# Kernel optimization log

Hardware: AMD Instinct MI355X
Metric: run time of the kernel (lower is better)

## Reference

```python
import jax, jax.numpy as jnp
import numpy as np

B, C, H, W = 2, 192, 48, 512
EMB, HEADS, DOUT, MAXM, THR, EPS = 64, 2, 192, 64, 0.01, 1e-5
DV = DOUT // HEADS  # per-head value dim (96)


def setup_inputs() -> dict:
    key = jax.random.key(0)
    ks = jax.random.split(key, 16)
    s = 0.02
    inp = {
        "l": jax.random.normal(ks[0], (B, C, H, W), jnp.float32),
        "r": jax.random.normal(ks[1], (B, C, H, W), jnp.float32),
        "ln_l_g": jnp.ones((C,), jnp.float32),
        "ln_l_b": jnp.zeros((C,), jnp.float32),
        "ln_r_g": jnp.ones((C,), jnp.float32),
        "ln_r_b": jnp.zeros((C,), jnp.float32),
    }
    ki = 2
    for p in ("rtl", "ltr"):
        inp[p + "_wq"] = jax.random.normal(ks[ki], (HEADS * EMB, C, 3), jnp.float32) * s; ki += 1
        inp[p + "_bq"] = jnp.zeros((HEADS * EMB,), jnp.float32)
        inp[p + "_wk"] = jax.random.normal(ks[ki], (HEADS * EMB, C, 3), jnp.float32) * s; ki += 1
        inp[p + "_bk"] = jnp.zeros((HEADS * EMB,), jnp.float32)
        inp[p + "_wv"] = jax.random.normal(ks[ki], (DOUT, C, 3), jnp.float32) * s; ki += 1
        inp[p + "_bv"] = jnp.zeros((DOUT,), jnp.float32)
        inp[p + "_wo"] = jax.random.normal(ks[ki], (DOUT, DOUT), jnp.float32) * s; ki += 1
        inp[p + "_bo"] = jnp.zeros((DOUT,), jnp.float32)
    inp["ffl_w"] = jax.random.normal(ks[ki], (DOUT, DOUT), jnp.float32) * s; ki += 1
    inp["ffl_b"] = jnp.zeros((DOUT,), jnp.float32)
    inp["ffr_w"] = jax.random.normal(ks[ki], (DOUT, DOUT), jnp.float32) * s; ki += 1
    inp["ffr_b"] = jnp.zeros((DOUT,), jnp.float32)
    return inp


def _layernorm(x, g, b):
    m = x.mean(-1, keepdims=True)
    v = x.var(-1, keepdims=True)
    return (x - m) / jnp.sqrt(v + EPS) * g + b


def _conv1d(x, w, b):
    # x: [N, Cin, L], w: [Cout, Cin, 3], same padding
    y = jax.lax.conv_general_dilated(x, w, (1,), [(1, 1)], dimension_numbers=("NCH", "OIH", "NCH"))
    return y + b[None, :, None]


def _conv_attn(q_seq, k_seq, v_seq, wq, bq, wk, bk, wv, bv, wo, bo, mask):
    # q_seq/k_seq/v_seq: [N, L, C]; mask: [L, L] bool (True = masked)
    N, L, _ = q_seq.shape
    Q = _conv1d(q_seq.transpose(0, 2, 1), wq, bq).reshape(N, HEADS, EMB, L).transpose(0, 1, 3, 2)  # b h l d
    K = _conv1d(k_seq.transpose(0, 2, 1), wk, bk).reshape(N, HEADS, EMB, L).transpose(0, 1, 3, 2)
    V = _conv1d(v_seq.transpose(0, 2, 1), wv, bv).reshape(N, HEADS, DV, L).transpose(0, 1, 3, 2)
    A = jnp.einsum("bhqd,bhkd->bhqk", Q, K) / np.sqrt(EMB).astype(np.float32)
    A = jnp.where(mask, -jnp.inf, A)
    A = jax.nn.softmax(A, axis=-1)
    A = A * (A > THR)  # valid_mask thresholding after softmax
    O = jnp.einsum("bhqk,bhkd->bhqd", A, V)
    O = O.transpose(0, 2, 1, 3).reshape(N, L, DOUT)
    return jnp.einsum("nld,od->nlo", O, wo) + bo, A


def reference(l, r, ln_l_g, ln_l_b, ln_r_g, ln_r_b,
              rtl_wq, rtl_bq, rtl_wk, rtl_bk, rtl_wv, rtl_bv, rtl_wo, rtl_bo,
              ltr_wq, ltr_bq, ltr_wk, ltr_bk, ltr_wv, ltr_bv, ltr_wo, ltr_bo,
              ffl_w, ffl_b, ffr_w, ffr_b):
    ls = l.transpose(0, 2, 3, 1).reshape(B * H, W, C)  # (b h) w c
    rs = r.transpose(0, 2, 3, 1).reshape(B * H, W, C)
    ln_ = _layernorm(ls, ln_l_g, ln_l_b)
    rn_ = _layernorm(rs, ln_r_g, ln_r_b)
    i = jnp.arange(W)[:, None]
    j = jnp.arange(W)[None, :]
    mask_left = (j < i) | (j - i > MAXM)   # left query i attends keys j in [i, i+MAXM]
    mask_right = (j > i) | (i - j > MAXM)  # right query i attends keys j in [i-MAXM, i]
    l_mha, A_rtl = _conv_attn(ln_, rn_, rs, rtl_wq, rtl_bq, rtl_wk, rtl_bk, rtl_wv, rtl_bv, rtl_wo, rtl_bo, mask_left)
    r_mha, A_ltr = _conv_attn(rn_, ln_, ls, ltr_wq, ltr_bq, ltr_wk, ltr_bk, ltr_wv, ltr_bv, ltr_wo, ltr_bo, mask_right)
    lo = ls + l_mha
    ro = rs + r_mha
    lo = lo + (jnp.einsum("nwc,oc->nwo", lo, ffl_w) + ffl_b)
    ro = ro + (jnp.einsum("nwc,oc->nwo", ro, ffr_w) + ffr_b)
    l_out = lo.reshape(B, H, W, C).transpose(0, 3, 1, 2)
    r_out = ro.reshape(B, H, W, C).transpose(0, 3, 1, 2)
    return (l_out, r_out, A_rtl, A_ltr)
```

## Files before the change

kernel.cpp:

```cpp
#include <hip/hip_runtime.h>
#include <cstddef>
#include <cstdint>

constexpr int kC = 192;
constexpr int kW = 512;
constexpr int kHH = 48;

typedef unsigned short u16;
typedef __attribute__((ext_vector_type(8))) short bf16x8;
typedef __attribute__((ext_vector_type(4))) float f32x4;
typedef __attribute__((ext_vector_type(4))) unsigned short us4;

__device__ inline u16 f2bf(float f) {
  union { float f; uint32_t u; } v; v.f = f;
  uint32_t r = v.u + 0x7FFF + ((v.u >> 16) & 1);
  return (u16)(r >> 16);
}
__device__ inline float bf2f(u16 u) {
  return __uint_as_float(((uint32_t)u) << 16);
}

__global__ void __launch_bounds__(256) prep_kernel(
    const float* __restrict__ xl, const float* __restrict__ xr,
    const float* __restrict__ gl, const float* __restrict__ bl,
    const float* __restrict__ gr, const float* __restrict__ br,
    u16* __restrict__ lnl, u16* __restrict__ lraw,
    u16* __restrict__ lnr, u16* __restrict__ rraw,
    const float* wq0, const float* wk0, const float* wv0,
    const float* wq1, const float* wk1, const float* wv1,
    const float* bq0, const float* bk0, const float* bv0,
    const float* bq1, const float* bk1, const float* bv1,
    const float* wo0, const float* wo1, const float* fw0, const float* fw1,
    u16* __restrict__ wall, u16* __restrict__ pfw, float* __restrict__ ball) {
  int bid = blockIdx.x;
  int tid = threadIdx.x;
  if (bid >= 1536) {
    int idx = (bid - 1536) * 256 + tid;
    if (idx < 516096) {
      int dir = idx / 258048, off = idx % 258048;
      const float* src; int soff;
      if (off < 73728) { src = dir ? wq1 : wq0; soff = off; }
      else if (off < 147456) { src = dir ? wk1 : wk0; soff = off - 73728; }
      else { src = dir ? wv1 : wv0; soff = off - 147456; }
      int o = soff / 576, k = soff % 576, t = k / 192, c = k % 192;
      wall[idx] = f2bf(src[((size_t)o * kC + c) * 3 + t]);
    } else if (idx < 516096 + 147456) {
      int i2 = idx - 516096;
      int mat = i2 / 36864, off = i2 % 36864;
      const float* src = mat == 0 ? wo0 : mat == 1 ? wo1 : mat == 2 ? fw0 : fw1;
      pfw[i2] = f2bf(src[off]);
    } else if (idx < 516096 + 147456 + 896) {
      int bi = idx - 516096 - 147456;
      int dir = bi / 448, boff = bi % 448;
      const float* s; int so;
      if (boff < 128) { s = dir ? bq1 : bq0; so = boff; }
      else if (boff < 256) { s = dir ? bk1 : bk0; so = boff - 128; }
      else { s = dir ? bv1 : bv0; so = boff - 256; }
      ball[bi] = s[so];
    }
    return;
  }
  int w0 = (bid & 7) * 64;
  int n = (bid >> 3) % 96;
  int side = bid / 768;
  const float* x = side ? xr : xl;
  const float* g = side ? gr : gl;
  const float* b = side ? br : bl;
  u16* lnout = side ? lnr : lnl;
  u16* rawout = side ? rraw : lraw;
  int bb = n / kHH, h = n % kHH;
  __shared__ float tile[64][193];
  __shared__ float red[8][64];
  __shared__ float mean_s[64], rstd_s[64];
  int lane = tid & 63, wv = tid >> 6;
  for (int c = wv; c < kC; c += 4)
    tile[lane][c] = x[(((size_t)bb * kC + c) * kHH + h) * kW + w0 + lane];
  __syncthreads();
  {
    int w = tid & 63, part = tid >> 6;
    float s = 0.f, s2 = 0.f;
    const float* row = &tile[w][0];
    for (int c = part * 48; c < part * 48 + 48; ++c) {
      float v = row[c];
      s += v; s2 += v * v;
    }
    red[part][w] = s;
    red[part + 4][w] = s2;
  }
  __syncthreads();
  if (tid < 64) {
    float s = red[0][tid] + red[1][tid] + red[2][tid] + red[3][tid];
    float s2 = red[4][tid] + red[5][tid] + red[6][tid] + red[7][tid];
    float m = s * (1.f / 192.f);
    float var = s2 * (1.f / 192.f) - m * m;
    mean_s[tid] = m;
    rstd_s[tid] = rsqrtf(var + 1e-5f);
  }
  __syncthreads();
  for (int u = tid; u < 64 * 48; u += 256) {
    int w = u / 48, c4 = (u % 48) * 4;
    float mm = mean_s[w], rs = rstd_s[w];
    us4 lp, rp;
#pragma unroll
    for (int j = 0; j < 4; ++j) {
      float raw = tile[w][c4 + j];
      rp[j] = f2bf(raw);
      lp[j] = f2bf((raw - mm) * rs * g[c4 + j] + b[c4 + j]);
    }
    size_t idx = ((size_t)n * kW + w0 + w) * kC + c4;
    *reinterpret_cast<us4*>(&lnout[idx]) = lp;
    *reinterpret_cast<us4*>(&rawout[idx]) = rp;
  }
}

template <int NF>
__device__ __forceinline__ void conv_core(
    const u16* __restrict__ in, const u16* __restrict__ w2,
    int n, int l0, u16* As, f32x4 (&acc)[4][NF]) {
  int tid = threadIdx.x;
  int wid = tid >> 6, lane = tid & 63;
  int wm = wid >> 1, wn = wid & 1;
  int lr = lane & 15, g = lane >> 4;
  for (int u = tid; u < 130 * 48; u += 256) {
    int row = u / 48, q = u % 48;
    int l = l0 - 1 + row;
    us4 v = {0, 0, 0, 0};
    if (l >= 0 && l < kW)
      v = *reinterpret_cast<const us4*>(in + ((size_t)n * kW + l) * kC + q * 4);
    *reinterpret_cast<us4*>(&As[row * 200 + q * 4]) = v;
  }
  __syncthreads();
  const u16* wbase = w2 + (size_t)(wn * NF * 16 + lr) * 576 + g * 8;
#pragma unroll
  for (int t = 0; t < 3; ++t) {
#pragma unroll
    for (int c0 = 0; c0 < 192; c0 += 64) {
#pragma unroll
      for (int ks = 0; ks < 2; ++ks) {
        bf16x8 a[4], b[NF];
#pragma unroll
        for (int mf = 0; mf < 4; ++mf)
          a[mf] = *reinterpret_cast<const bf16x8*>(
              &As[(wm * 64 + mf * 16 + lr + t) * 200 + c0 + ks * 32 + g * 8]);
#pragma unroll
        for (int nf = 0; nf < NF; ++nf)
          b[nf] = *reinterpret_cast<const bf16x8*>(
              wbase + (size_t)nf * 16 * 576 + t * 192 + c0 + ks * 32);
#pragma unroll
        for (int mf = 0; mf < 4; ++mf)
#pragma unroll
          for (int nf = 0; nf < NF; ++nf)
            acc[mf][nf] = __builtin_amdgcn_mfma_f32_16x16x32_bf16(a[mf], b[nf], acc[mf][nf], 0, 0, 0);
      }
    }
  }
}

__global__ void __launch_bounds__(256) conv_qk(
    const u16* __restrict__ lnl, const u16* __restrict__ lnr,
    const u16* __restrict__ wall, const float* __restrict__ ball,
    u16* __restrict__ Qbf, u16* __restrict__ Kbf, float* __restrict__ A0) {
  if (blockIdx.y == 4) {
    int fid = blockIdx.z * 4 + blockIdx.x;
    int base_row = fid * 256;
    f32x4 z4 = {0.f, 0.f, 0.f, 0.f};
    for (int u = threadIdx.x; u < 256 * 128; u += 256) {
      int lrow = u >> 7, c4 = u & 127;
      int rg = base_row + lrow;
      int nh = rg >> 9, i = rg & 511;
      int q0 = i & ~63;
      int w1 = q0 + 128 > 512 ? 512 : q0 + 128;
      int col = c4 * 4;
      if (col < q0 || col >= w1)
        __builtin_nontemporal_store(z4, reinterpret_cast<f32x4*>(
            A0 + (size_t)nh * 262144 + (size_t)i * 512 + col));
    }
    return;
  }
  int l0 = blockIdx.x * 128;
  int jid = blockIdx.y;
  int n = blockIdx.z;
  int dir = jid >> 1, which = jid & 1;
  const u16* in = which == 0 ? (dir ? lnr : lnl) : (dir ? lnl : lnr);
  const u16* w2 = wall + (size_t)dir * 258048 + which * 73728;
  const float* bias = ball + dir * 448 + which * 128;

  __shared__ __attribute__((aligned(16))) u16 As[130 * 200];
  f32x4 acc[4][4] = {};
  conv_core<4>(in, w2, n, l0, As, acc);

  int tid = threadIdx.x;
  int wid = tid >> 6, lane = tid & 63;
  int wm = wid >> 1, wn = wid & 1;
  int lr = lane & 15, g = lane >> 4;
  __syncthreads();
  u16* Ts = As;
#pragma unroll
  for (int nf = 0; nf < 4; ++nf) {
    int o = wn * 64 + nf * 16 + lr;
    float bsv = bias[o];
#pragma unroll
    for (int mf = 0; mf < 4; ++mf) {
      int lbase = wm * 64 + mf * 16 + g * 4;
#pragma unroll
      for (int rg = 0; rg < 4; ++rg)
        Ts[(lbase + rg) * 132 + o] = f2bf(acc[mf][nf][rg] + bsv);
    }
  }
  __syncthreads();
  u16* outp = (which == 0 ? Qbf : Kbf) + (size_t)dir * 6291456;
  for (int u = tid; u < 4096; u += 256) {
    int hh = u >> 11;
    int rem = u & 2047;
    int l = rem >> 4, q4 = (rem & 15) * 4;
    us4 v = *reinterpret_cast<const us4*>(&Ts[l * 132 + hh * 64 + q4]);
    *reinterpret_cast<us4*>(
        &outp[((size_t)(n * 2 + hh) * kW + l0 + l) * 64 + q4]) = v;
  }
}

__global__ void __launch_bounds__(256) conv_v(
    const u16* __restrict__ lraw, const u16* __restrict__ rraw,
    const u16* __restrict__ wall, const float* __restrict__ ball,
    u16* __restrict__ Vbf, float* __restrict__ A1) {
  if (blockIdx.y == 2) {
    int fid = blockIdx.z * 4 + blockIdx.x;
    int base_row = fid * 256;
    f32x4 z4 = {0.f, 0.f, 0.f, 0.f};
    for (int u = threadIdx.x; u < 256 * 128; u += 256) {
      int lrow = u >> 7, c4 = u & 127;
      int rg = base_row + lrow;
      int nh = rg >> 9, i = rg & 511;
      int q0 = i & ~63;
      int w0 = q0 >= 64 ? q0 - 64 : 0;
      int col = c4 * 4;
      if (col < w0 || col >= q0 + 64)
        __builtin_nontemporal_store(z4, reinterpret_cast<f32x4*>(
            A1 + (size_t)nh * 262144 + (size_t)i * 512 + col));
    }
    return;
  }
  int l0 = blockIdx.x * 128;
  int dir = blockIdx.y;
  int n = blockIdx.z;
  const u16* in = dir ? lraw : rraw;
  const u16* w2 = wall + (size_t)dir * 258048 + 147456;
  const float* bias = ball + dir * 448 + 256;

  __shared__ __attribute__((aligned(16))) u16 As[130 * 200];
  f32x4 acc[4][6] = {};
  conv_core<6>(in, w2, n, l0, As, acc);

  int tid = threadIdx.x;
  int wid = tid >> 6, lane = tid & 63;
  int wm = wid >> 1, wn = wid & 1;
  int lr = lane & 15, g = lane >> 4;
  u16* outp = Vbf + (size_t)dir * 9437184;
#pragma unroll
  for (int nf = 0; nf < 6; ++nf) {
    int e = nf * 16 + lr;
    float bsv = bias[wn * 96 + e];
#pragma unroll
    for (int mf = 0; mf < 4; ++mf) {
      int lb = l0 + wm * 64 + mf * 16 + g * 4;
      us4 p;
#pragma unroll
      for (int rg = 0; rg < 4; ++rg) p[rg] = f2bf(acc[mf][nf][rg] + bsv);
      *reinterpret_cast<us4*>(&outp[((size_t)(n * 2 + wn) * 96 + e) * kW + lb]) = p;
    }
  }
}

__global__ void __launch_bounds__(256) attn_projff(
    const u16* __restrict__ Qbf, const u16* __restrict__ Kbf,
    const u16* __restrict__ Vbf, const u16* __restrict__ pfw,
    const float* __restrict__ bo0, const float* __restrict__ bo1,
    const float* __restrict__ fb0, const float* __restrict__ fb1,
    const u16* __restrict__ lraw, const u16* __restrict__ rraw,
    float* __restrict__ Abase, float* __restrict__ outbase) {
  int qb = blockIdx.x;
  int n = blockIdx.y;
  int dir = blockIdx.z;
  int q0 = qb * 64;
  int k_start = dir == 0 ? q0 : (q0 >= 64 ? q0 - 64 : 0);
  int k_end = dir == 0 ? (q0 + 128 <= kW ? q0 + 128 : kW) : q0 + 64;
  int kfr = (k_end - k_start) >> 4;

  __shared__ __attribute__((aligned(16))) u16 smem[35072];
  u16* Ks = smem;
  u16* Ps = smem;
  u16* Vt = smem + 9216;
  u16* Rs = smem;
  u16* Os = smem + 22272;

  int tid = threadIdx.x;
  int wid = tid >> 6, lane = tid & 63;
  int lr = lane & 15, g = lane >> 4;

  int lo_k = q0 + wid * 16 - (dir == 0 ? 0 : 64) - k_start;
  int hi_k = q0 + wid * 16 + 15 + (dir == 0 ? 64 : 0) - k_start;
  int i = q0 + wid * 16 + lr;

#pragma unroll
  for (int h = 0; h < 2; ++h) {
    int nh = n * 2 + h;
    const u16* Q = Qbf + ((size_t)dir * 192 + nh) * kW * 64;
    const u16* K = Kbf + ((size_t)dir * 192 + nh) * kW * 64;
    const u16* V = Vbf + ((size_t)dir * 192 + nh) * 96 * kW;
    float* Aout = Abase + (size_t)dir * 50331648 + (size_t)nh * 262144;

    for (int u = tid; u < 128 * 16; u += 256) {
      int row = u >> 4, c4 = (u & 15) * 4;
      *reinterpret_cast<us4*>(&Ks[row * 72 + c4]) =
          *reinterpret_cast<const us4*>(&K[(size_t)(k_start + row) * 64 + c4]);
    }
    for (int u = tid; u < 96 * 32; u += 256) {
      int row = u >> 5, c4 = (u & 31) * 4;
      *reinterpret_cast<us4*>(&Vt[row * 136 + c4]) =
          *reinterpret_cast<const us4*>(&V[(size_t)row * kW + k_start + c4]);
    }
    const u16* Qrow = Q + (size_t)(q0 + wid * 16 + lr) * 64 + g * 8;
    bf16x8 bq0 = *reinterpret_cast<const bf16x8*>(Qrow);
    bf16x8 bq1 = *reinterpret_cast<const bf16x8*>(Qrow + 32);
    __syncthreads();

    f32x4 sT[8];
#pragma unroll
    for (int kf = 0; kf < 8; ++kf) sT[kf] = f32x4{0.f, 0.f, 0.f, 0.f};
#pragma unroll
    for (int kf = 0; kf < 8; ++kf) {
      if (kf * 16 + 15 >= lo_k && kf * 16 <= hi_k) {
        bf16x8 ak0 = *reinterpret_cast<const bf16x8*>(&Ks[(kf * 16 + lr) * 72 + g * 8]);
        sT[kf] = __builtin_amdgcn_mfma_f32_16x16x32_bf16(ak0, bq0, sT[kf], 0, 0, 0);
        bf16x8 ak1 = *reinterpret_cast<const bf16x8*>(&Ks[(kf * 16 + lr) * 72 + 32 + g * 8]);
        sT[kf] = __builtin_amdgcn_mfma_f32_16x16x32_bf16(ak1, bq1, sT[kf], 0, 0, 0);
      }
    }

    float mx = -INFINITY;
#pragma unroll
    for (int kf = 0; kf < 8; ++kf) {
#pragma unroll
      for (int r = 0; r < 4; ++r) {
        int jj = k_start + kf * 16 + g * 4 + r;
        bool valid = (jj < k_end) &&
                     (dir == 0 ? (jj >= i && jj - i <= 64) : (jj <= i && i - jj <= 64));
        float v = valid ? sT[kf][r] * 0.125f : -INFINITY;
        sT[kf][r] = v;
        mx = fmaxf(mx, v);
      }
    }
    mx = fmaxf(mx, __shfl_xor(mx, 16));
    mx = fmaxf(mx, __shfl_xor(mx, 32));
    float ssum = 0.f;
#pragma unroll
    for (int kf = 0; kf < 8; ++kf) {
#pragma unroll
      for (int r = 0; r < 4; ++r) {
        float e = __expf(sT[kf][r] - mx);
        sT[kf][r] = e;
        ssum += e;
      }
    }
    ssum += __shfl_xor(ssum, 16);
    ssum += __shfl_xor(ssum, 32);
    float inv = 1.f / ssum;

    __syncthreads();

    {
      float* arow = Aout + (size_t)i * kW + k_start;
#pragma unroll
      for (int kf = 0; kf < 8; ++kf) {
        f32x4 pv;
        us4 pb;
#pragma unroll
        for (int r = 0; r < 4; ++r) {
          float p = sT[kf][r] * inv;
          p = (p > 0.01f) ? p : 0.f;
          pv[r] = p;
          pb[r] = f2bf(p);
        }
        *reinterpret_cast<us4*>(&Ps[(wid * 16 + lr) * 136 + kf * 16 + g * 4]) = pb;
        if (kf < kfr)
          __builtin_nontemporal_store(pv, reinterpret_cast<f32x4*>(arow + kf * 16 + g * 4));
      }
    }
    __syncthreads();

    f32x4 oacc[6];
#pragma unroll
    for (int ef = 0; ef < 6; ++ef) oacc[ef] = f32x4{0.f, 0.f, 0.f, 0.f};
#pragma unroll
    for (int kc = 0; kc < 4; ++kc) {
      if (kc * 32 + 31 >= lo_k && kc * 32 <= hi_k) {
        bf16x8 ap = *reinterpret_cast<const bf16x8*>(&Ps[(wid * 16 + lr) * 136 + kc * 32 + g * 8]);
#pragma unroll
        for (int ef = 0; ef < 6; ++ef) {
          bf16x8 bv = *reinterpret_cast<const bf16x8*>(&Vt[(ef * 16 + lr) * 136 + kc * 32 + g * 8]);
          oacc[ef] = __builtin_amdgcn_mfma_f32_16x16x32_bf16(ap, bv, oacc[ef], 0, 0, 0);
        }
      }
    }
#pragma unroll
    for (int ef = 0; ef < 6; ++ef) {
      int e = h * 96 + ef * 16 + lr;
#pragma unroll
      for (int r = 0; r < 4; ++r)
        Os[(wid * 16 + g * 4 + r) * 200 + e] = f2bf(oacc[ef][r]);
    }
    __syncthreads();
  }

  const u16* resbf = dir ? rraw : lraw;
  for (int u = tid; u < 64 * 48; u += 256) {
    int row = u / 48, q = u % 48;
    *reinterpret_cast<us4*>(&Rs[row * 200 + q * 4]) =
        *reinterpret_cast<const us4*>(&resbf[((size_t)n * kW + q0 + row) * kC + q * 4]);
  }

  const u16* wo2 = pfw + (dir ? 36864 : 0);
  const u16* fw2 = pfw + 73728 + (dir ? 36864 : 0);
  const float* bo_ = dir ? bo1 : bo0;
  const float* fb_ = dir ? fb1 : fb0;
  float* outb = outbase + (size_t)dir * 9437184;
  int bb = n / kHH, hh_ = n % kHH;

  int wm = wid >> 1, wn = wid & 1;
  const u16* wobase = wo2 + (size_t)(wn * 96 + lr) * kC + g * 8;
  const u16* fwbase = fw2 + (size_t)(wn * 96 + lr) * kC + g * 8;

  f32x4 accp[2][6] = {};
#pragma unroll
  for (int c0 = 0; c0 < 192; c0 += 64) {
#pragma unroll
    for (int ks = 0; ks < 2; ++ks) {
      bf16x8 a[2], b[6];
#pragma unroll
      for (int m2 = 0; m2 < 2; ++m2)
        a[m2] = *reinterpret_cast<const bf16x8*>(
            &Os[(wm * 32 + m2 * 16 + lr) * 200 + c0 + ks * 32 + g * 8]);
#pragma unroll
      for (int nf = 0; nf < 6; ++nf)
        b[nf] = *reinterpret_cast<const bf16x8*>(
            wobase + (size_t)nf * 16 * kC + c0 + ks * 32);
#pragma unroll
      for (int m2 = 0; m2 < 2; ++m2)
#pragma unroll
        for (int nf = 0; nf < 6; ++nf)
          accp[m2][nf] = __builtin_amdgcn_mfma_f32_16x16x32_bf16(a[m2], b[nf], accp[m2][nf], 0, 0, 0);
    }
  }
  __syncthreads();
#pragma unroll
  for (int nf = 0; nf < 6; ++nf) {
    int o = wn * 96 + nf * 16 + lr;
    float bv = bo_[o];
#pragma unroll
    for (int m2 = 0; m2 < 2; ++m2) {
#pragma unroll
      for (int r = 0; r < 4; ++r) {
        int l = wm * 32 + m2 * 16 + g * 4 + r;
        float v = accp[m2][nf][r] + bv + bf2f(Rs[l * 200 + o]);
        accp[m2][nf][r] = v;
        Os[l * 200 + o] = f2bf(v);
      }
    }
  }
  __syncthreads();

  f32x4 accf[2][6] = {};
#pragma unroll
  for (int c0 = 0; c0 < 192; c0 += 64) {
#pragma unroll
    for (int ks = 0; ks < 2; ++ks) {
      bf16x8 a[2], b[6];
#pragma unroll
      for (int m2 = 0; m2 < 2; ++m2)
        a[m2] = *reinterpret_cast<const bf16x8*>(
            &Os[(wm * 32 + m2 * 16 + lr) * 200 + c0 + ks * 32 + g * 8]);
#pragma unroll
      for (int nf = 0; nf < 6; ++nf)
        b[nf] = *reinterpret_cast<const bf16x8*>(
            fwbase + (size_t)nf * 16 * kC + c0 + ks * 32);
#pragma unroll
      for (int m2 = 0; m2 < 2; ++m2)
#pragma unroll
        for (int nf = 0; nf < 6; ++nf)
          accf[m2][nf] = __builtin_amdgcn_mfma_f32_16x16x32_bf16(a[m2], b[nf], accf[m2][nf], 0, 0, 0);
    }
  }
#pragma unroll
  for (int nf = 0; nf < 6; ++nf) {
    int o = wn * 96 + nf * 16 + lr;
    float bv = fb_[o];
#pragma unroll
    for (int m2 = 0; m2 < 2; ++m2) {
      f32x4 ov;
#pragma unroll
      for (int r = 0; r < 4; ++r)
        ov[r] = accf[m2][nf][r] + bv + accp[m2][nf][r];
      int l = q0 + wm * 32 + m2 * 16 + g * 4;
      *reinterpret_cast<f32x4*>(&outb[(((size_t)bb * kC + o) * kHH + hh_) * kW + l]) = ov;
    }
  }
}

extern "C" void kernel_launch(void* const* d_in, const int* in_sizes, int n_in,
                              void* d_out, int out_size, void* d_ws, size_t ws_size,
                              hipStream_t stream) {
  const float* l = (const float*)d_in[0];
  const float* r = (const float*)d_in[1];
  float* out = (float*)d_out;
  float* ws = (float*)d_ws;

  u16* lnl_bf  = (u16*)(ws + 0);
  u16* lnr_bf  = (u16*)(ws + 4718592);
  u16* lraw_bf = (u16*)(ws + 9437184);
  u16* rraw_bf = (u16*)(ws + 14155776);
  u16* wall    = (u16*)(ws + 18874368);
  float* ball  = ws + 19136512;
  u16* Qbf     = (u16*)(ws + 19137536);
  u16* Kbf     = (u16*)(ws + 25428992);
  u16* Vbf     = (u16*)(ws + 31720448);
  u16* pfw     = (u16*)(ws + 50594816);

  float* A0 = out + (size_t)18874368;
  float* A1 = out + (size_t)69206016;

  int wp_items = 516096 + 147456 + 896;
  int wp_blocks = (wp_items + 255) / 256;
  prep_kernel<<<1536 + wp_blocks, 256, 0, stream>>>(
      l, r, (const float*)d_in[2], (const float*)d_in[3],
      (const float*)d_in[4], (const float*)d_in[5],
      lnl_bf, lraw_bf, lnr_bf, rraw_bf,
      (const float*)d_in[6], (const float*)d_in[8], (const float*)d_in[10],
      (const float*)d_in[14], (const float*)d_in[16], (const float*)d_in[18],
      (const float*)d_in[7], (const float*)d_in[9], (const float*)d_in[11],
      (const float*)d_in[15], (const float*)d_in[17], (const float*)d_in[19],
      (const float*)d_in[12], (const float*)d_in[20],
      (const float*)d_in[22], (const float*)d_in[24],
      wall, pfw, ball);

  conv_qk<<<dim3(4, 5, 96), 256, 0, stream>>>(
      lnl_bf, lnr_bf, wall, ball, Qbf, Kbf, A0);
  conv_v<<<dim3(4, 3, 96), 256, 0, stream>>>(
      lraw_bf, rraw_bf, wall, ball, Vbf, A1);

  attn_projff<<<dim3(8, 96, 2), 256, 0, stream>>>(
      Qbf, Kbf, Vbf, pfw,
      (const float*)d_in[13], (const float*)d_in[21],
      (const float*)d_in[23], (const float*)d_in[25],
      lraw_bf, rraw_bf, A0, out);
}
```

Baseline: 348.3 us.

## Prefetch second head's K, V, Q into registers during first head

During the first head iteration, the attention kernel now issues global loads for the second head's K, V and Q tiles into registers (20 us4 plus two bf16x8 per thread). In the second iteration it writes them to shared memory from registers instead of loading from global. The aim is to overlap the second head's global-load latency with the first head's compute. The extra registers raise register pressure and could lower occupancy or cause spills.

```diff
diff --git a/kernel.cpp b/kernel.cpp
--- a/kernel.cpp
+++ b/kernel.cpp
@@ -301,6 +301,9 @@
   int hi_k = q0 + wid * 16 + 15 + (dir == 0 ? 64 : 0) - k_start;
   int i = q0 + wid * 16 + lr;
 
+  us4 kpre[8], vpre[12];
+  bf16x8 bq0_1, bq1_1;
+
 #pragma unroll
   for (int h = 0; h < 2; ++h) {
     int nh = n * 2 + h;
@@ -309,19 +312,55 @@
     const u16* V = Vbf + ((size_t)dir * 192 + nh) * 96 * kW;
     float* Aout = Abase + (size_t)dir * 50331648 + (size_t)nh * 262144;
 
-    for (int u = tid; u < 128 * 16; u += 256) {
-      int row = u >> 4, c4 = (u & 15) * 4;
-      *reinterpret_cast<us4*>(&Ks[row * 72 + c4]) =
-          *reinterpret_cast<const us4*>(&K[(size_t)(k_start + row) * 64 + c4]);
-    }
-    for (int u = tid; u < 96 * 32; u += 256) {
-      int row = u >> 5, c4 = (u & 31) * 4;
-      *reinterpret_cast<us4*>(&Vt[row * 136 + c4]) =
-          *reinterpret_cast<const us4*>(&V[(size_t)row * kW + k_start + c4]);
-    }
-    const u16* Qrow = Q + (size_t)(q0 + wid * 16 + lr) * 64 + g * 8;
-    bf16x8 bq0 = *reinterpret_cast<const bf16x8*>(Qrow);
-    bf16x8 bq1 = *reinterpret_cast<const bf16x8*>(Qrow + 32);
+    bf16x8 bq0, bq1;
+    if (h == 0) {
+      for (int u = tid; u < 128 * 16; u += 256) {
+        int row = u >> 4, c4 = (u & 15) * 4;
+        *reinterpret_cast<us4*>(&Ks[row * 72 + c4]) =
+            *reinterpret_cast<const us4*>(&K[(size_t)(k_start + row) * 64 + c4]);
+      }
+      for (int u = tid; u < 96 * 32; u += 256) {
+        int row = u >> 5, c4 = (u & 31) * 4;
+        *reinterpret_cast<us4*>(&Vt[row * 136 + c4]) =
+            *reinterpret_cast<const us4*>(&V[(size_t)row * kW + k_start + c4]);
+      }
+      const u16* Qrow = Q + (size_t)(q0 + wid * 16 + lr) * 64 + g * 8;
+      bq0 = *reinterpret_cast<const bf16x8*>(Qrow);
+      bq1 = *reinterpret_cast<const bf16x8*>(Qrow + 32);
+      const u16* K1 = Kbf + ((size_t)dir * 192 + n * 2 + 1) * kW * 64;
+      const u16* V1 = Vbf + ((size_t)dir * 192 + n * 2 + 1) * 96 * kW;
+      const u16* Q1 = Qbf + ((size_t)dir * 192 + n * 2 + 1) * kW * 64;
+#pragma unroll
+      for (int j = 0; j < 8; ++j) {
+        int u = tid + j * 256;
+        int row = u >> 4, c4 = (u & 15) * 4;
+        kpre[j] = *reinterpret_cast<const us4*>(&K1[(size_t)(k_start + row) * 64 + c4]);
+      }
+#pragma unroll
+      for (int j = 0; j < 12; ++j) {
+        int u = tid + j * 256;
+        int row = u >> 5, c4 = (u & 31) * 4;
+        vpre[j] = *reinterpret_cast<const us4*>(&V1[(size_t)row * kW + k_start + c4]);
+      }
+      const u16* Q1row = Q1 + (size_t)(q0 + wid * 16 + lr) * 64 + g * 8;
+      bq0_1 = *reinterpret_cast<const bf16x8*>(Q1row);
+      bq1_1 = *reinterpret_cast<const bf16x8*>(Q1row + 32);
+    } else {
+#pragma unroll
+      for (int j = 0; j < 8; ++j) {
+        int u = tid + j * 256;
+        int row = u >> 4, c4 = (u & 15) * 4;
+        *reinterpret_cast<us4*>(&Ks[row * 72 + c4]) = kpre[j];
+      }
+#pragma unroll
+      for (int j = 0; j < 12; ++j) {
+        int u = tid + j * 256;
+        int row = u >> 5, c4 = (u & 31) * 4;
+        *reinterpret_cast<us4*>(&Vt[row * 136 + c4]) = vpre[j];
+      }
+      bq0 = bq0_1;
+      bq1 = bq1_1;
+    }
     __syncthreads();
 
     f32x4 sT[8];
```

Measured after the change: 396.3 us. 1.14x slower.
